# Performance work log

Hardware: AMD Instinct MI355X
Metric: run time of the kernel (lower is better)

The kernel has to match this reference:

```python
import math
import jax, jax.numpy as jnp
import numpy as np

D_MODEL = 1024
N_HEAD = 16
D_HEAD = 64
Q_LEN = 2048
MEM_LEN = 2048
K_LEN = MEM_LEN + Q_LEN
B = 1
LN_EPS = 1e-5


def setup_inputs() -> dict:
    key = jax.random.key(0)
    ks = jax.random.split(key, 8)
    hidden = jax.random.normal(ks[0], (B, Q_LEN, D_MODEL), dtype=jnp.float32)
    position_embedding = jax.random.normal(ks[1], (K_LEN, D_MODEL), dtype=jnp.float32)
    u = jax.random.normal(ks[2], (N_HEAD, D_HEAD), dtype=jnp.float32) * 0.02
    v = jax.random.normal(ks[3], (N_HEAD, D_HEAD), dtype=jnp.float32) * 0.02
    memory = jax.random.normal(ks[4], (B, MEM_LEN, D_MODEL), dtype=jnp.float32)
    # TXL causal mask: query i may attend to key j iff j <= i + MEM_LEN
    i = jnp.arange(Q_LEN)[:, None]
    j = jnp.arange(K_LEN)[None, :]
    mask = (j > (i + MEM_LEN))[None, None]  # (1,1,Q,K) bool, True = masked
    # weights (torch Linear has no bias here); stored as (in, out)
    s = 1.0 / math.sqrt(D_MODEL)
    W_qkv = jax.random.normal(ks[5], (D_MODEL, 3 * N_HEAD * D_HEAD), dtype=jnp.float32) * s
    W_pe = jax.random.normal(ks[6], (D_MODEL, N_HEAD * D_HEAD), dtype=jnp.float32) * s
    W_out = jax.random.normal(ks[7], (N_HEAD * D_HEAD, D_MODEL), dtype=jnp.float32) * (1.0 / math.sqrt(N_HEAD * D_HEAD))
    return {"hidden": hidden, "position_embedding": position_embedding, "u": u,
            "v": v, "mask": mask, "memory": memory,
            "W_qkv": W_qkv, "W_pe": W_pe, "W_out": W_out}


def _layer_norm(x):
    # elementwise_affine=False LayerNorm over last dim
    mu = jnp.mean(x, axis=-1, keepdims=True)
    var = jnp.var(x, axis=-1, keepdims=True)
    return (x - mu) / jnp.sqrt(var + LN_EPS)


def reference(hidden, position_embedding, u, v, mask, memory, W_qkv, W_pe, W_out):
    batch, q_len, _ = hidden.shape
    k_len = position_embedding.shape[0]
    scale = 1.0 / math.sqrt(D_HEAD)

    mh = jnp.concatenate([memory, hidden], axis=1)          # (B, k_len, d_model)
    qkv = mh @ W_qkv                                        # post-norm: no LN on input
    Q, K, V = jnp.split(qkv, 3, axis=-1)
    Q = Q[:, -q_len:, :]
    pe = position_embedding @ W_pe                          # (k_len, H*D)

    Q = Q.reshape(batch, q_len, N_HEAD, D_HEAD)
    K = K.reshape(batch, k_len, N_HEAD, D_HEAD)
    V = V.reshape(batch, k_len, N_HEAD, D_HEAD)
    pe = pe.reshape(batch, k_len, N_HEAD, D_HEAD)

    AC = jnp.einsum('bqhd,bkhd->bhqk', Q + u, K)
    BD = jnp.einsum('bqhd,bkhd->bhqk', Q + v, pe)
    # NOTE: the original module calls relative_shift(BD) but DISCARDS the
    # result, so BD is used unshifted. We faithfully reproduce that.
    score = (AC + BD) * scale
    score = jnp.where(mask, -jnp.inf, score)
    prob = jax.nn.softmax(score, axis=-1)                   # (B,H,Q,K)
    av = jnp.einsum('bhqk,bkhd->bqhd', prob, V)
    av = av.reshape(batch, q_len, N_HEAD * D_HEAD)
    attn_out = av @ W_out
    return _layer_norm(hidden + attn_out)                   # post-norm residual
```

## Files before the change

kernel.cpp:

```cpp
#include <hip/hip_runtime.h>

typedef __attribute__((ext_vector_type(4))) float f32x4;
typedef __attribute__((ext_vector_type(16))) float f32x16;
typedef __attribute__((ext_vector_type(8))) short bf16x8;
typedef __attribute__((ext_vector_type(4))) unsigned short u16x4;
typedef unsigned short u16;

#define DM 1024
#define NHEAD 16
#define DHEAD 64
#define QLEN 2048
#define MLEN 2048
#define KLEN 4096
#define QSCALE 0.18033688011112042f

__device__ __forceinline__ float bf2f(u16 u) {
    unsigned i = ((unsigned)u) << 16; float f; __builtin_memcpy(&f, &i, 4); return f;
}
__device__ __forceinline__ u16 f2bf(float f) {
    unsigned i; __builtin_memcpy(&i, &f, 4);
    unsigned r = i + 0x7fffu + ((i >> 16) & 1u);
    return (u16)(r >> 16);
}
__device__ __forceinline__ float exp2_fast(float x) {
#if __has_builtin(__builtin_amdgcn_exp2f)
    return __builtin_amdgcn_exp2f(x);
#else
    return exp2f(x);
#endif
}
__device__ __forceinline__ unsigned cvtpk_bf16(float lo, float hi) {
    unsigned r;
    asm("v_cvt_pk_bf16_f32 %0, %1, %2" : "=v"(r) : "v"(lo), "v"(hi));
    return r;
}
__device__ __forceinline__ void gl2lds16(const void* g, void* l) {
    __builtin_amdgcn_global_load_lds((const __attribute__((address_space(1))) void*)g,
                                     (__attribute__((address_space(3))) void*)l, 16, 0, 0);
}

__global__ __launch_bounds__(256) void prep(
    const float* __restrict__ memory, const float* __restrict__ hidden,
    const float* __restrict__ pos, const float* __restrict__ Wqkv,
    const float* __restrict__ Wpe, const float* __restrict__ Wout,
    u16* __restrict__ MH, u16* __restrict__ PEA,
    u16* __restrict__ WQKVT, u16* __restrict__ WPET, u16* __restrict__ WOUTT)
{
    __shared__ float ls[64][65];
    const int b = blockIdx.x, t = threadIdx.x;
    if (b < 8192) {
        size_t e = ((size_t)b * 256 + t) * 4;
        const size_t HALF = (size_t)KLEN * DM;
        f32x4 v; u16* dst;
        if (e < HALF) {
            size_t row = e >> 10, col = e & 1023;
            const float* src = (row < MLEN) ? (memory + row * DM) : (hidden + (row - MLEN) * DM);
            v = *(const f32x4*)(src + col);
            dst = MH + e;
        } else {
            size_t e2 = e - HALF;
            v = *(const f32x4*)(pos + e2);
            dst = PEA + e2;
        }
        u16x4 o;
        #pragma unroll
        for (int c = 0; c < 4; ++c) o[c] = f2bf(v[c]);
        *(u16x4*)dst = o;
        return;
    }
    int tb = b - 8192;
    const float* src; u16* dst; int N, bx, by;
    if (tb < 768)       { src = Wqkv; dst = WQKVT; N = 3 * DM; bx = tb % 48; by = tb / 48; }
    else if (tb < 1024) { int i = tb - 768;  src = Wpe;  dst = WPET;  N = DM; bx = i & 15; by = i >> 4; }
    else                { int i = tb - 1024; src = Wout; dst = WOUTT; N = DM; bx = i & 15; by = i >> 4; }
    const int n0 = bx * 64, k0 = by * 64;
    const int c = t & 63, rg = t >> 6;
    #pragma unroll
    for (int p = 0; p < 16; ++p) {
        int r = p * 4 + rg;
        ls[r][c] = src[(size_t)(k0 + r) * N + n0 + c];
    }
    __syncthreads();
    #pragma unroll
    for (int p = 0; p < 16; ++p) {
        int r = p * 4 + rg;
        dst[(size_t)(n0 + r) * DM + k0 + c] = f2bf(ls[c][r]);
    }
}

__global__ __launch_bounds__(256, 3) void gemm_qkvpe(
    const u16* __restrict__ MH, const u16* __restrict__ PEA,
    const u16* __restrict__ WQKVT, const u16* __restrict__ WPET,
    const float* __restrict__ u, const float* __restrict__ vv,
    u16* __restrict__ QHAT, u16* __restrict__ KHAT, u16* __restrict__ VB)
{
    __shared__ u16 lsA[128 * 64];
    __shared__ u16 lsB[128 * 64];
    const int b = blockIdx.x;
    int row0, col0, region; const u16 *A, *B;
    if (b < 512)      { row0 = (b >> 4) * 128; col0 = 1024 + (b & 15) * 128; A = MH; B = WQKVT;
                        region = (col0 < 2048) ? 1 : 2; }
    else if (b < 640) { int i = b - 512; row0 = 2048 + (i >> 3) * 128; col0 = (i & 7) * 128;
                        A = MH; B = WQKVT; region = 0; }
    else              { int i = b - 640; row0 = (i >> 3) * 128; col0 = (i & 7) * 128;
                        A = PEA; B = WPET; region = 3; }
    const int tid = threadIdx.x, wave = tid >> 6, lane = tid & 63;
    const int blk = lane >> 4, ln = lane & 15;
    const int wr = (wave >> 1) << 6, wc = (wave & 1) << 6;
    const int rstage = lane >> 3;
    const int cswz = ((lane & 7) ^ rstage) * 8;

    f32x4 acc[4][4];
    #pragma unroll
    for (int i = 0; i < 4; ++i)
        #pragma unroll
        for (int j = 0; j < 4; ++j) acc[i][j] = f32x4{0.f, 0.f, 0.f, 0.f};

    for (int k0 = 0; k0 < DM; k0 += 64) {
        #pragma unroll
        for (int t = 0; t < 4; ++t) {
            int chunk = wave * 4 + t;
            int r = chunk * 8 + rstage;
            gl2lds16(A + (size_t)(row0 + r) * DM + k0 + cswz, lsA + chunk * 512);
            gl2lds16(B + (size_t)(col0 + r) * DM + k0 + cswz, lsB + chunk * 512);
        }
        __syncthreads();
        #pragma unroll
        for (int kk = 0; kk < 2; ++kk) {
            bf16x8 af[4], bfr[4];
            #pragma unroll
            for (int i = 0; i < 4; ++i) {
                int ro = wr + i * 16 + ln;
                af[i] = *(const bf16x8*)(lsA + ro * 64 + (((kk * 4 + blk) ^ (ro & 7)) * 8));
            }
            #pragma unroll
            for (int j = 0; j < 4; ++j) {
                int ro = wc + j * 16 + ln;
                bfr[j] = *(const bf16x8*)(lsB + ro * 64 + (((kk * 4 + blk) ^ (ro & 7)) * 8));
            }
            #pragma unroll
            for (int i = 0; i < 4; ++i)
                #pragma unroll
                for (int j = 0; j < 4; ++j)
                    acc[i][j] = __builtin_amdgcn_mfma_f32_16x16x32_bf16(af[i], bfr[j], acc[i][j], 0, 0, 0);
        }
        __syncthreads();
    }
    #pragma unroll
    for (int i = 0; i < 4; ++i)
        #pragma unroll
        for (int j = 0; j < 4; ++j)
            #pragma unroll
            for (int r = 0; r < 4; ++r) {
                int row = row0 + wr + i * 16 + blk * 4 + r;
                int col = col0 + wc + j * 16 + ln;
                float val = acc[i][j][r];
                if (region == 0) {
                    int q = row - MLEN, h = col >> 6;
                    size_t base = ((size_t)h * QLEN + q) * 128 + (col & 63);
                    QHAT[base]      = f2bf((val + u[col]) * QSCALE);
                    QHAT[base + 64] = f2bf((val + vv[col]) * QSCALE);
                } else if (region == 1) {
                    int c = col - 1024, h = c >> 6;
                    KHAT[((size_t)h * KLEN + row) * 128 + (c & 63)] = f2bf(val);
                } else if (region == 2) {
                    VB[(size_t)row * DM + (col - 2048)] = f2bf(val);
                } else {
                    int h = col >> 6;
                    KHAT[((size_t)h * KLEN + row) * 128 + 64 + (col & 63)] = f2bf(val);
                }
            }
}

__global__ __launch_bounds__(256) void pack_vt(const u16* __restrict__ VB, u16* __restrict__ VT)
{
    __shared__ float ls[64][65];
    const int kt = blockIdx.x, h = blockIdx.y;
    const int t = threadIdx.x, c = t & 63, rg = t >> 6;
    #pragma unroll
    for (int p = 0; p < 16; ++p) {
        int r = p * 4 + rg;
        ls[r][c] = bf2f(VB[(size_t)(kt * 64 + r) * DM + h * 64 + c]);
    }
    __syncthreads();
    #pragma unroll
    for (int p = 0; p < 16; ++p) {
        int d = p * 4 + rg;
        VT[((size_t)h * DHEAD + d) * KLEN + kt * 64 + c] = f2bf(ls[c][d]);
    }
}

__global__ __launch_bounds__(256, 4) void attn_fused(
    const u16* __restrict__ QHAT, const u16* __restrict__ KHAT,
    const u16* __restrict__ VT, u16* __restrict__ OPb, float* __restrict__ ML)
{
    __shared__ __align__(16) u16 smem[18432];
    const int b = blockIdx.x;
    const int h  = ((b & 7) << 1) | ((b >> 3) & 1);
    const int ks = b >> 8;
    const int qb = (((b >> 4) & 15) + 4 * ks) & 15;
    const int tid = threadIdx.x;
    const int wave = tid >> 6, lane = tid & 63;
    const int l31 = lane & 31, hi = lane >> 5;
    const int qrow0 = qb * 128 + wave * 32;
    u16* pb = smem + 13312 + wave * 1280;
    const int px = (l31 >> 3) & 3;

    const u16* khp = KHAT + (size_t)h * KLEN * 128;
    const u16* vhp = VT + (size_t)h * DHEAD * KLEN;

    const int nt = qb + 17;
    const int kbase = ks * nt * 32;
    const int vd = tid >> 2, vc = tid & 3;
    const int vslot = vc ^ ((vd >> 3) & 3);

    auto stage_load = [&](int buf, int kt) -> bf16x8 {
        const int k0 = kbase + kt * 32;
        u16* Kb = smem + buf * 4096;
        #pragma unroll
        for (int i = 0; i < 2; ++i) {
            int c = i * 256 + tid;
            int row = c >> 4, cgl = c & 15;
            int cs = cgl ^ (row & 15);
            gl2lds16(khp + ((size_t)(k0 + row) << 7) + cs * 8,
                     Kb + (size_t)(i * 256 + (tid & ~63)) * 8);
        }
        return *(const bf16x8*)(vhp + (size_t)vd * KLEN + k0 + vc * 8);
    };
    auto stage_write = [&](int buf, bf16x8 vr) {
        *(bf16x8*)(smem + 8192 + buf * 2560 + vd * 40 + vslot * 8) = vr;
    };

    bf16x8 qf[8];
    {
        const u16* qbase = QHAT + ((size_t)h * QLEN + qrow0 + l31) * 128 + hi * 8;
        #pragma unroll
        for (int kd = 0; kd < 8; ++kd) qf[kd] = *(const bf16x8*)(qbase + kd * 16);
    }

    f32x16 oacc[2];
    #pragma unroll
    for (int dg = 0; dg < 2; ++dg)
        #pragma unroll
        for (int r = 0; r < 16; ++r) oacc[dg][r] = 0.f;
    float mi = -1e30f, li = 0.f;

    const int qlim = qrow0 + 31 + MLEN;
    const int qsel = qrow0 + l31 + MLEN;

    bf16x8 vreg = stage_load(0, 0);
    asm volatile("s_waitcnt vmcnt(0)" ::: "memory");
    stage_write(0, vreg);
    __syncthreads();

    int cur = 0;
    for (int kt = 0; kt < nt; ++kt) {
        const int k0 = kbase + kt * 32;
        const bool pre = (kt + 1 < nt);
        if (pre) vreg = stage_load(cur ^ 1, kt + 1);

        if (k0 <= qlim) {
            f32x16 sacc;
            #pragma unroll
            for (int r = 0; r < 16; ++r) sacc[r] = 0.f;
            const u16* kb = smem + cur * 4096;
            const int rx = l31 & 15;
            #pragma unroll
            for (int kd = 0; kd < 8; ++kd) {
                int cd = (kd * 2 + hi) ^ rx;
                bf16x8 kf = *(const bf16x8*)(kb + l31 * 128 + cd * 8);
                sacc = __builtin_amdgcn_mfma_f32_32x32x16_bf16(kf, qf[kd], sacc, 0, 0, 0);
            }
            if (k0 + 31 > qrow0 + MLEN) {
                const int keyb = k0 + 4 * hi;
                #pragma unroll
                for (int r = 0; r < 16; ++r) {
                    int key = keyb + (r & 3) + 8 * (r >> 2);
                    if (key > qsel) sacc[r] = -1e30f;
                }
            }
            float mt;
            {
                f32x4 m4;
                #pragma unroll
                for (int r = 0; r < 4; ++r)
                    m4[r] = fmaxf(fmaxf(sacc[r], sacc[4 + r]), fmaxf(sacc[8 + r], sacc[12 + r]));
                mt = fmaxf(fmaxf(m4[0], m4[1]), fmaxf(m4[2], m4[3]));
            }
            mt = fmaxf(mt, __shfl_xor(mt, 32, 64));
            if (!__all(mt <= mi + 8.f)) {
                float mn = fmaxf(mi, mt);
                float corr = exp2_fast(mi - mn);
                mi = mn;
                li *= corr;
                #pragma unroll
                for (int dg = 0; dg < 2; ++dg)
                    #pragma unroll
                    for (int r = 0; r < 16; ++r) oacc[dg][r] *= corr;
            }
            #pragma unroll
            for (int r = 0; r < 16; ++r) sacc[r] = exp2_fast(sacc[r] - mi);
            float rs;
            {
                f32x4 s4;
                #pragma unroll
                for (int r = 0; r < 4; ++r)
                    s4[r] = (sacc[r] + sacc[4 + r]) + (sacc[8 + r] + sacc[12 + r]);
                rs = (s4[0] + s4[1]) + (s4[2] + s4[3]);
            }
            li += rs + __shfl_xor(rs, 32, 64);
            {
                unsigned* pd = (unsigned*)(pb + (size_t)l31 * 40);
                #pragma unroll
                for (int b2 = 0; b2 < 4; ++b2)
                    #pragma unroll
                    for (int c = 0; c < 2; ++c)
                        pd[(b2 ^ px) * 4 + 2 * hi + c] =
                            cvtpk_bf16(sacc[4 * b2 + 2 * c], sacc[4 * b2 + 2 * c + 1]);
            }
            #pragma unroll
            for (int kkl = 0; kkl < 2; ++kkl) {
                bf16x8 pf = *(const bf16x8*)(pb + (size_t)l31 * 40 + ((kkl * 2 + hi) ^ px) * 8);
                #pragma unroll
                for (int dg = 0; dg < 2; ++dg) {
                    int vrow = dg * 32 + l31;
                    int cd = (kkl * 2 + hi) ^ ((l31 >> 3) & 3);
                    bf16x8 vf = *(const bf16x8*)(smem + 8192 + cur * 2560 + vrow * 40 + cd * 8);
                    oacc[dg] = __builtin_amdgcn_mfma_f32_32x32x16_bf16(vf, pf, oacc[dg], 0, 0, 0);
                }
            }
        }
        asm volatile("s_waitcnt vmcnt(0)" ::: "memory");
        if (pre) stage_write(cur ^ 1, vreg);
        __syncthreads();
        cur ^= 1;
    }

    const int q = qrow0 + l31;
    unsigned* op32 = (unsigned*)(OPb + (((size_t)ks * QLEN + q) * NHEAD + h) * 64);
    #pragma unroll
    for (int dg = 0; dg < 2; ++dg) {
        union { f32x16 v; float f[16]; } oo;
        oo.v = oacc[dg];
        #pragma unroll
        for (int b2 = 0; b2 < 4; ++b2)
            #pragma unroll
            for (int c = 0; c < 2; ++c)
                op32[(dg * 32 + 8 * b2 + 4 * hi) / 2 + c] =
                    cvtpk_bf16(oo.f[4 * b2 + 2 * c], oo.f[4 * b2 + 2 * c + 1]);
    }
    if (!hi) {
        float* ml = ML + (((size_t)ks * QLEN + q) * NHEAD + h) * 2;
        ml[0] = mi; ml[1] = li;
    }
}

__global__ __launch_bounds__(256) void attn_combine(
    const u16* __restrict__ OPb, const float* __restrict__ ML, u16* __restrict__ AVB)
{
    int idx = blockIdx.x * 256 + threadIdx.x;
    int d8 = (idx & 7) * 8;
    int h  = (idx >> 3) & 15;
    int q  = idx >> 7;
    float m[4], l[4], mf = -1e30f;
    #pragma unroll
    for (int ks = 0; ks < 4; ++ks) {
        const float* ml = ML + (((size_t)ks * QLEN + q) * NHEAD + h) * 2;
        m[ks] = ml[0]; l[ks] = ml[1];
        mf = fmaxf(mf, m[ks]);
    }
    float lsum = 0.f;
    float a[4];
    #pragma unroll
    for (int ks = 0; ks < 4; ++ks) {
        a[ks] = exp2_fast(m[ks] - mf);
        lsum += a[ks] * l[ks];
    }
    float inv = 1.f / lsum;
    float acc[8];
    #pragma unroll
    for (int j = 0; j < 8; ++j) acc[j] = 0.f;
    #pragma unroll
    for (int ks = 0; ks < 4; ++ks) {
        float w = a[ks] * inv;
        const u16* src = OPb + (((size_t)ks * QLEN + q) * NHEAD + h) * 64 + d8;
        u16x4 x0 = *(const u16x4*)(src);
        u16x4 x1 = *(const u16x4*)(src + 4);
        #pragma unroll
        for (int j = 0; j < 4; ++j) { acc[j] += w * bf2f(x0[j]); acc[4 + j] += w * bf2f(x1[j]); }
    }
    unsigned* A32 = (unsigned*)AVB;
    size_t base = ((size_t)q * DM + h * 64 + d8) >> 1;
    #pragma unroll
    for (int j = 0; j < 4; ++j)
        A32[base + j] = cvtpk_bf16(acc[2 * j], acc[2 * j + 1]);
}

__global__ __launch_bounds__(256, 3) void gemm_out(
    const u16* __restrict__ A, const u16* __restrict__ Bt, float* __restrict__ RES)
{
    __shared__ u16 lsA[128 * 64];
    __shared__ u16 lsB[128 * 64];
    const int b = blockIdx.x;
    const int tile = b >> 1, kh = b & 1;
    const int row0 = (tile >> 3) * 128, col0 = (tile & 7) * 128;
    const int tid = threadIdx.x, wave = tid >> 6, lane = tid & 63;
    const int blk = lane >> 4, ln = lane & 15;
    const int wr = (wave >> 1) << 6, wc = (wave & 1) << 6;
    const int rstage = lane >> 3;
    const int cswz = ((lane & 7) ^ rstage) * 8;

    f32x4 acc[4][4];
    #pragma unroll
    for (int i = 0; i < 4; ++i)
        #pragma unroll
        for (int j = 0; j < 4; ++j) acc[i][j] = f32x4{0.f, 0.f, 0.f, 0.f};

    for (int k0 = kh * 512; k0 < kh * 512 + 512; k0 += 64) {
        #pragma unroll
        for (int t = 0; t < 4; ++t) {
            int chunk = wave * 4 + t;
            int r = chunk * 8 + rstage;
            gl2lds16(A  + (size_t)(row0 + r) * DM + k0 + cswz, lsA + chunk * 512);
            gl2lds16(Bt + (size_t)(col0 + r) * DM + k0 + cswz, lsB + chunk * 512);
        }
        __syncthreads();
        #pragma unroll
        for (int kk = 0; kk < 2; ++kk) {
            bf16x8 af[4], bfr[4];
            #pragma unroll
            for (int i = 0; i < 4; ++i) {
                int ro = wr + i * 16 + ln;
                af[i] = *(const bf16x8*)(lsA + ro * 64 + (((kk * 4 + blk) ^ (ro & 7)) * 8));
            }
            #pragma unroll
            for (int j = 0; j < 4; ++j) {
                int ro = wc + j * 16 + ln;
                bfr[j] = *(const bf16x8*)(lsB + ro * 64 + (((kk * 4 + blk) ^ (ro & 7)) * 8));
            }
            #pragma unroll
            for (int i = 0; i < 4; ++i)
                #pragma unroll
                for (int j = 0; j < 4; ++j)
                    acc[i][j] = __builtin_amdgcn_mfma_f32_16x16x32_bf16(af[i], bfr[j], acc[i][j], 0, 0, 0);
        }
        __syncthreads();
    }
    float* C = RES + (size_t)kh * QLEN * DM;
    #pragma unroll
    for (int i = 0; i < 4; ++i)
        #pragma unroll
        for (int j = 0; j < 4; ++j)
            #pragma unroll
            for (int r = 0; r < 4; ++r) {
                int row = row0 + wr + i * 16 + blk * 4 + r;
                int col = col0 + wc + j * 16 + ln;
                C[(size_t)row * DM + col] = acc[i][j][r];
            }
}

__global__ __launch_bounds__(256) void ln_kernel(
    const float* __restrict__ hidden, const float* __restrict__ RES, float* __restrict__ out)
{
    const int row = blockIdx.x, t = threadIdx.x;
    const int wave = t >> 6, lane = t & 63;
    __shared__ float ws[8];
    f32x4 a = ((const f32x4*)(hidden + (size_t)row * DM))[t];
    f32x4 r0 = ((const f32x4*)(RES + (size_t)row * DM))[t];
    f32x4 r1 = ((const f32x4*)(RES + (size_t)(QLEN + row) * DM))[t];
    f32x4 v;
    #pragma unroll
    for (int c = 0; c < 4; ++c) v[c] = a[c] + r0[c] + r1[c];
    float s = v[0] + v[1] + v[2] + v[3];
    float s2 = v[0] * v[0] + v[1] * v[1] + v[2] * v[2] + v[3] * v[3];
    #pragma unroll
    for (int off = 1; off < 64; off <<= 1) {
        s += __shfl_xor(s, off, 64);
        s2 += __shfl_xor(s2, off, 64);
    }
    if (lane == 0) { ws[wave] = s; ws[4 + wave] = s2; }
    __syncthreads();
    float ts = ws[0] + ws[1] + ws[2] + ws[3];
    float ts2 = ws[4] + ws[5] + ws[6] + ws[7];
    float mu = ts * (1.f / DM);
    float var = ts2 * (1.f / DM) - mu * mu;
    float rsq = rsqrtf(var + 1e-5f);
    f32x4 o;
    #pragma unroll
    for (int c = 0; c < 4; ++c) o[c] = (v[c] - mu) * rsq;
    ((f32x4*)(out + (size_t)row * DM))[t] = o;
}

extern "C" void kernel_launch(void* const* d_in, const int* in_sizes, int n_in,
                              void* d_out, int out_size, void* d_ws, size_t ws_size,
                              hipStream_t stream)
{
    const float* hidden = (const float*)d_in[0];
    const float* pos    = (const float*)d_in[1];
    const float* u      = (const float*)d_in[2];
    const float* vv     = (const float*)d_in[3];
    const float* memory = (const float*)d_in[5];
    const float* Wqkv   = (const float*)d_in[6];
    const float* Wpe    = (const float*)d_in[7];
    const float* Wout   = (const float*)d_in[8];
    float* out = (float*)d_out;

    char* w = (char*)d_ws;
    auto alloc = [&](size_t bytes) {
        void* p = (void*)w;
        w += (bytes + 255) & ~(size_t)255;
        return p;
    };
    u16* MH    = (u16*)alloc((size_t)KLEN * DM * 2);
    u16* PEA   = (u16*)alloc((size_t)KLEN * DM * 2);
    u16* WQKVT = (u16*)alloc((size_t)3 * DM * DM * 2);
    u16* WPET  = (u16*)alloc((size_t)DM * DM * 2);
    u16* VB    = (u16*)alloc((size_t)KLEN * DM * 2);
    u16* QHAT  = (u16*)alloc((size_t)NHEAD * QLEN * 128 * 2);
    u16* KHAT  = (u16*)alloc((size_t)NHEAD * KLEN * 128 * 2);
    u16* VTb   = (u16*)alloc((size_t)NHEAD * DHEAD * KLEN * 2);
    u16* AVB   = (u16*)alloc((size_t)QLEN * DM * 2);
    float* RES = (float*)alloc((size_t)2 * QLEN * DM * 4);
    u16* WOUTT = (u16*)alloc((size_t)DM * DM * 2);
    u16* OPb   = (u16*)d_ws;
    float* ML  = (float*)((char*)d_ws + (size_t)4 * QLEN * NHEAD * 64 * 2);

    prep<<<8192 + 1280, 256, 0, stream>>>(memory, hidden, pos, Wqkv, Wpe, Wout,
                                          MH, PEA, WQKVT, WPET, WOUTT);
    gemm_qkvpe<<<896, 256, 0, stream>>>(MH, PEA, WQKVT, WPET, u, vv, QHAT, KHAT, VB);
    pack_vt<<<dim3(KLEN / 64, NHEAD), 256, 0, stream>>>(VB, VTb);
    attn_fused<<<dim3(1024), 256, 0, stream>>>(QHAT, KHAT, VTb, OPb, ML);
    attn_combine<<<dim3(QLEN * NHEAD * 8 / 256), 256, 0, stream>>>(OPb, ML, AVB);
    gemm_out<<<256, 256, 0, stream>>>(AVB, WOUTT, RES);
    ln_kernel<<<QLEN, 256, 0, stream>>>(hidden, RES, out);
}
```

Before: 162.1 us.

## Double-buffer LDS in projection GEMMs and raise MFMA wave priority in attention

Both projection GEMMs (QKV/PE and output) now use two LDS buffers: they issue global-to-LDS loads for the next K step before computing on the current one. This overlaps memory latency with MFMA work and drops one barrier per iteration. LDS per block doubles to 64KB, so occupancy falls from 3 to 2 blocks per CU. The attention kernel also wraps its two MFMA loops in s_setprio(1) to favour the matrix-issuing waves.

```diff
diff --git a/kernel.cpp b/kernel.cpp
--- a/kernel.cpp
+++ b/kernel.cpp
@@ -88,14 +88,13 @@
     }
 }
 
-__global__ __launch_bounds__(256, 3) void gemm_qkvpe(
+__global__ __launch_bounds__(256, 2) void gemm_qkvpe(
     const u16* __restrict__ MH, const u16* __restrict__ PEA,
     const u16* __restrict__ WQKVT, const u16* __restrict__ WPET,
     const float* __restrict__ u, const float* __restrict__ vv,
     u16* __restrict__ QHAT, u16* __restrict__ KHAT, u16* __restrict__ VB)
 {
-    __shared__ u16 lsA[128 * 64];
-    __shared__ u16 lsB[128 * 64];
+    __shared__ __align__(16) u16 ls[2][2 * 8192];
     const int b = blockIdx.x;
     int row0, col0, region; const u16 *A, *B;
     if (b < 512)      { row0 = (b >> 4) * 128; col0 = 1024 + (b & 15) * 128; A = MH; B = WQKVT;
@@ -110,33 +109,43 @@
     const int rstage = lane >> 3;
     const int cswz = ((lane & 7) ^ rstage) * 8;
 
-    f32x4 acc[4][4];
-    #pragma unroll
-    for (int i = 0; i < 4; ++i)
-        #pragma unroll
-        for (int j = 0; j < 4; ++j) acc[i][j] = f32x4{0.f, 0.f, 0.f, 0.f};
-
-    for (int k0 = 0; k0 < DM; k0 += 64) {
+    auto stage = [&](int buf, int k0) {
         #pragma unroll
         for (int t = 0; t < 4; ++t) {
             int chunk = wave * 4 + t;
             int r = chunk * 8 + rstage;
-            gl2lds16(A + (size_t)(row0 + r) * DM + k0 + cswz, lsA + chunk * 512);
-            gl2lds16(B + (size_t)(col0 + r) * DM + k0 + cswz, lsB + chunk * 512);
-        }
-        __syncthreads();
+            gl2lds16(A + (size_t)(row0 + r) * DM + k0 + cswz, &ls[buf][chunk * 512]);
+            gl2lds16(B + (size_t)(col0 + r) * DM + k0 + cswz, &ls[buf][8192 + chunk * 512]);
+        }
+    };
+
+    f32x4 acc[4][4];
+    #pragma unroll
+    for (int i = 0; i < 4; ++i)
+        #pragma unroll
+        for (int j = 0; j < 4; ++j) acc[i][j] = f32x4{0.f, 0.f, 0.f, 0.f};
+
+    stage(0, 0);
+    asm volatile("s_waitcnt vmcnt(0)" ::: "memory");
+    __syncthreads();
+    int cur = 0;
+    const int NSTEP = 16;
+    for (int t = 0; t < NSTEP; ++t) {
+        if (t + 1 < NSTEP) stage(cur ^ 1, (t + 1) * 64);
+        const u16* la = ls[cur];
+        const u16* lb = ls[cur] + 8192;
         #pragma unroll
         for (int kk = 0; kk < 2; ++kk) {
             bf16x8 af[4], bfr[4];
             #pragma unroll
             for (int i = 0; i < 4; ++i) {
                 int ro = wr + i * 16 + ln;
-                af[i] = *(const bf16x8*)(lsA + ro * 64 + (((kk * 4 + blk) ^ (ro & 7)) * 8));
+                af[i] = *(const bf16x8*)(la + ro * 64 + (((kk * 4 + blk) ^ (ro & 7)) * 8));
             }
             #pragma unroll
             for (int j = 0; j < 4; ++j) {
                 int ro = wc + j * 16 + ln;
-                bfr[j] = *(const bf16x8*)(lsB + ro * 64 + (((kk * 4 + blk) ^ (ro & 7)) * 8));
+                bfr[j] = *(const bf16x8*)(lb + ro * 64 + (((kk * 4 + blk) ^ (ro & 7)) * 8));
             }
             #pragma unroll
             for (int i = 0; i < 4; ++i)
@@ -144,8 +153,11 @@
                 for (int j = 0; j < 4; ++j)
                     acc[i][j] = __builtin_amdgcn_mfma_f32_16x16x32_bf16(af[i], bfr[j], acc[i][j], 0, 0, 0);
         }
+        asm volatile("s_waitcnt vmcnt(0)" ::: "memory");
         __syncthreads();
-    }
+        cur ^= 1;
+    }
+
     #pragma unroll
     for (int i = 0; i < 4; ++i)
         #pragma unroll
@@ -265,12 +277,14 @@
             for (int r = 0; r < 16; ++r) sacc[r] = 0.f;
             const u16* kb = smem + cur * 4096;
             const int rx = l31 & 15;
+            __builtin_amdgcn_s_setprio(1);
             #pragma unroll
             for (int kd = 0; kd < 8; ++kd) {
                 int cd = (kd * 2 + hi) ^ rx;
                 bf16x8 kf = *(const bf16x8*)(kb + l31 * 128 + cd * 8);
                 sacc = __builtin_amdgcn_mfma_f32_32x32x16_bf16(kf, qf[kd], sacc, 0, 0, 0);
             }
+            __builtin_amdgcn_s_setprio(0);
             if (k0 + 31 > qrow0 + MLEN) {
                 const int keyb = k0 + 4 * hi;
                 #pragma unroll
@@ -318,6 +332,7 @@
                         pd[(b2 ^ px) * 4 + 2 * hi + c] =
                             cvtpk_bf16(sacc[4 * b2 + 2 * c], sacc[4 * b2 + 2 * c + 1]);
             }
+            __builtin_amdgcn_s_setprio(1);
             #pragma unroll
             for (int kkl = 0; kkl < 2; ++kkl) {
                 bf16x8 pf = *(const bf16x8*)(pb + (size_t)l31 * 40 + ((kkl * 2 + hi) ^ px) * 8);
@@ -329,6 +344,7 @@
                     oacc[dg] = __builtin_amdgcn_mfma_f32_32x32x16_bf16(vf, pf, oacc[dg], 0, 0, 0);
                 }
             }
+            __builtin_amdgcn_s_setprio(0);
         }
         asm volatile("s_waitcnt vmcnt(0)" ::: "memory");
         if (pre) stage_write(cur ^ 1, vreg);
@@ -396,11 +412,10 @@
         A32[base + j] = cvtpk_bf16(acc[2 * j], acc[2 * j + 1]);
 }
 
-__global__ __launch_bounds__(256, 3) void gemm_out(
+__global__ __launch_bounds__(256, 2) void gemm_out(
     const u16* __restrict__ A, const u16* __restrict__ Bt, float* __restrict__ RES)
 {
-    __shared__ u16 lsA[128 * 64];
-    __shared__ u16 lsB[128 * 64];
+    __shared__ __align__(16) u16 ls[2][2 * 8192];
     const int b = blockIdx.x;
     const int tile = b >> 1, kh = b & 1;
     const int row0 = (tile >> 3) * 128, col0 = (tile & 7) * 128;
@@ -409,34 +424,45 @@
     const int wr = (wave >> 1) << 6, wc = (wave & 1) << 6;
     const int rstage = lane >> 3;
     const int cswz = ((lane & 7) ^ rstage) * 8;
-
-    f32x4 acc[4][4];
-    #pragma unroll
-    for (int i = 0; i < 4; ++i)
-        #pragma unroll
-        for (int j = 0; j < 4; ++j) acc[i][j] = f32x4{0.f, 0.f, 0.f, 0.f};
-
-    for (int k0 = kh * 512; k0 < kh * 512 + 512; k0 += 64) {
+    const int kbase = kh * 512;
+
+    auto stage = [&](int buf, int k0) {
         #pragma unroll
         for (int t = 0; t < 4; ++t) {
             int chunk = wave * 4 + t;
             int r = chunk * 8 + rstage;
-            gl2lds16(A  + (size_t)(row0 + r) * DM + k0 + cswz, lsA + chunk * 512);
-            gl2lds16(Bt + (size_t)(col0 + r) * DM + k0 + cswz, lsB + chunk * 512);
-        }
-        __syncthreads();
+            gl2lds16(A  + (size_t)(row0 + r) * DM + k0 + cswz, &ls[buf][chunk * 512]);
+            gl2lds16(Bt + (size_t)(col0 + r) * DM + k0 + cswz, &ls[buf][8192 + chunk * 512]);
+        }
+    };
+
+    f32x4 acc[4][4];
+    #pragma unroll
+    for (int i = 0; i < 4; ++i)
+        #pragma unroll
+        for (int j = 0; j < 4; ++j) acc[i][j] = f32x4{0.f, 0.f, 0.f, 0.f};
+
+    stage(0, kbase);
+    asm volatile("s_waitcnt vmcnt(0)" ::: "memory");
+    __syncthreads();
+    int cur = 0;
+    const int NSTEP = 8;
+    for (int t = 0; t < NSTEP; ++t) {
+        if (t + 1 < NSTEP) stage(cur ^ 1, kbase + (t + 1) * 64);
+        const u16* la = ls[cur];
+        const u16* lb = ls[cur] + 8192;
         #pragma unroll
         for (int kk = 0; kk < 2; ++kk) {
             bf16x8 af[4], bfr[4];
             #pragma unroll
             for (int i = 0; i < 4; ++i) {
                 int ro = wr + i * 16 + ln;
-                af[i] = *(const bf16x8*)(lsA + ro * 64 + (((kk * 4 + blk) ^ (ro & 7)) * 8));
+                af[i] = *(const bf16x8*)(la + ro * 64 + (((kk * 4 + blk) ^ (ro & 7)) * 8));
             }
             #pragma unroll
             for (int j = 0; j < 4; ++j) {
                 int ro = wc + j * 16 + ln;
-                bfr[j] = *(const bf16x8*)(lsB + ro * 64 + (((kk * 4 + blk) ^ (ro & 7)) * 8));
+                bfr[j] = *(const bf16x8*)(lb + ro * 64 + (((kk * 4 + blk) ^ (ro & 7)) * 8));
             }
             #pragma unroll
             for (int i = 0; i < 4; ++i)
@@ -444,7 +470,9 @@
                 for (int j = 0; j < 4; ++j)
                     acc[i][j] = __builtin_amdgcn_mfma_f32_16x16x32_bf16(af[i], bfr[j], acc[i][j], 0, 0, 0);
         }
+        asm volatile("s_waitcnt vmcnt(0)" ::: "memory");
         __syncthreads();
+        cur ^= 1;
     }
     float* C = RES + (size_t)kh * QLEN * DM;
     #pragma unroll
```

Result: no change. 162.3 us (+0.1%).
